# Kernel tuning notes

Hardware: AMD Instinct MI355X
Metric: run time of the kernel (lower is better)

Reference implementation:

```python
import jax, jax.numpy as jnp
import numpy as np

LINHAS, COLUNAS, DIM, BATCH = 64, 64, 512, 256
N_NEURONS = LINHAS * COLUNAS
TAXA_INICIAL = 0.5
SIGMA_INICIAL = max(LINHAS, COLUNAS) / 2.0  # 32.0


def _grid_locations():
    # Matches tf.meshgrid (default 'xy' indexing) -> stack -> reshape(-1, 2)
    x = jnp.arange(LINHAS, dtype=jnp.float32)
    y = jnp.arange(COLUNAS, dtype=jnp.float32)
    gx, gy = jnp.meshgrid(x, y)  # 'xy' indexing, shapes (COLUNAS, LINHAS)
    return jnp.stack([gx, gy], axis=-1).reshape(-1, 2)  # (N_NEURONS, 2)


def setup_inputs() -> dict:
    key = jax.random.key(0)
    kx, kw = jax.random.split(key)
    X = jax.random.normal(kx, (BATCH, DIM), dtype=jnp.float32)
    # keras 'random_normal' initializer: stddev 0.05
    pesos = jax.random.normal(kw, (N_NEURONS, DIM), dtype=jnp.float32) * 0.05
    return {
        "X": X,
        "pesos": pesos,
        "localizacoes": _grid_locations(),
        "passo_atual": 10,
        "total_passos": 1000,
    }


def reference(X, pesos, localizacoes, passo_atual, total_passos):
    decay = jnp.exp(jnp.float32(-passo_atual / total_passos))
    taxa = TAXA_INICIAL * decay
    sigma = SIGMA_INICIAL * decay

    # Euclidean cdist^2: (B, N)
    x2 = jnp.sum(X * X, axis=1, keepdims=True)            # (B, 1)
    w2 = jnp.sum(pesos * pesos, axis=1)                   # (N,)
    dist = x2 + w2 - 2.0 * (X @ pesos.T)                  # (B, N)

    bmu_idx = jnp.argmin(dist, axis=1)                    # (B,)
    bmu_loc = localizacoes[bmu_idx]                       # (B, 2)

    # Squared grid distance from every neuron to each sample's BMU: (B, N)
    diff = localizacoes[None, :, :] - bmu_loc[:, None, :]
    dist_grade = jnp.sum(diff * diff, axis=2)
    h = jnp.exp(-dist_grade / (2.0 * sigma * sigma))      # (B, N)

    # delta_total[n, d] = taxa * mean_b h[b, n] * (X[b, d] - pesos[n, d])
    # computed without materializing the (B, N, D) delta tensor.
    B = jnp.float32(X.shape[0])
    hX = jnp.einsum("bn,bd->nd", h, X)                    # (N, D)
    h_sum = jnp.sum(h, axis=0)                            # (N,)
    delta_total = (taxa / B) * (hX - h_sum[:, None] * pesos)

    new_pesos = pesos + delta_total
    return new_pesos, taxa, sigma
```

## Files before the change

kernel.cpp:

```cpp
#include <hip/hip_runtime.h>
#include <hip/hip_bf16.h>

typedef unsigned int u32;
typedef unsigned short u16;
typedef unsigned long long u64;

#define BATCH 256
#define NN 4096
#define DIM 512

using short8 = __attribute__((ext_vector_type(8))) short;
using f32x4  = __attribute__((ext_vector_type(4))) float;

__device__ inline float b2f(u16 u){ u32 i = ((u32)u)<<16; float f; __builtin_memcpy(&f,&i,4); return f; }
__device__ inline u16 f2b(float v){ __hip_bfloat16 h = __float2bfloat16(v); u16 r; __builtin_memcpy(&r,&h,2); return r; }

__device__ inline float ldv(const void* p, size_t i, int isbf){
  return isbf ? b2f(((const u16*)p)[i]) : ((const float*)p)[i];
}
__device__ inline void stv(void* p, size_t i, float v, int isbf){
  if (isbf) ((__hip_bfloat16*)p)[i] = __float2bfloat16(v);
  else ((float*)p)[i] = v;
}

__device__ inline int sniff(const void* X, int t, int* sh){
  if (t < 64){
    u32 v = ((const u32*)X)[t];
    u16 lo = (u16)(v & 0xffffu);
    int e = (lo >> 7) & 0xff;
    int sane = ((lo & 0x7fffu) == 0) || (e >= 110 && e <= 132);
    u64 m = __ballot(sane);
    if (t == 0) *sh = (__popcll(m) >= 32) ? 1 : 0;
  }
  __syncthreads();
  return *sh;
}

__global__ __launch_bounds__(256) void k_prep(const void* X, const void* W,
    u64* pack, float* w2, u16* XT, u16* Xb, u16* Wb,
    const int* passo, const int* total, void* out){
  __shared__ int sflag;
  __shared__ u32 sT[64][33];
  int t = threadIdx.x;
  int isbf = sniff(X, t, &sflag);
  int blk = blockIdx.x;
  if (blk < 32){
    int td = blk & 7, tb = blk >> 3;
    #pragma unroll
    for (int it=0; it<8; ++it){
      int i = it*256 + t;
      int r = i>>5, cc = i&31;
      size_t gi = (size_t)(tb*64 + r)*DIM + td*64 + cc*2;
      u32 v;
      if (isbf){
        v = *(const u32*)((const u16*)X + gi);
      } else {
        float2 f = *(const float2*)((const float*)X + gi);
        v = (u32)f2b(f.x) | ((u32)f2b(f.y) << 16);
        *(u32*)(Xb + gi) = v;
      }
      sT[r][cc] = v;
    }
    __syncthreads();
    #pragma unroll
    for (int it=0; it<8; ++it){
      int i = it*256 + t;
      int dd = i>>5, bb2 = i&31;
      u32 lo = sT[bb2*2][dd>>1], hi = sT[bb2*2+1][dd>>1];
      int sh = (dd&1)*16;
      u32 v = ((lo >> sh) & 0xffffu) | (((hi >> sh) & 0xffffu) << 16);
      *(u32*)(XT + (size_t)(td*64+dd)*BATCH + tb*64 + bb2*2) = v;
    }
  } else {
    int j = blk - 32;
    int n0 = j*8;
    int wv = t>>6, lane = t&63;
    #pragma unroll
    for (int rr=0; rr<2; ++rr){
      int n = n0 + wv*2 + rr;
      float xv[8]; float s = 0.f;
      if (isbf){
        short8 x = *(const short8*)((const u16*)W + (size_t)n*DIM + lane*8);
        #pragma unroll
        for (int q=0;q<8;q++) xv[q] = b2f((u16)x[q]);
      } else {
        #pragma unroll
        for (int q=0;q<8;q++) xv[q] = ((const float*)W)[(size_t)n*DIM + lane*8 + q];
      }
      #pragma unroll
      for (int q=0;q<8;q++) s += xv[q]*xv[q];
      #pragma unroll
      for (int off=32; off; off>>=1) s += __shfl_down(s, off);
      if (lane == 0) w2[n] = s;
      if (!isbf){
        #pragma unroll
        for (int q=0;q<8;q++) Wb[(size_t)n*DIM + lane*8 + q] = f2b(xv[q]);
      }
    }
    if (j == 0){
      pack[t] = ~0ull;
      if (t == 0){
        float decay = expf(-(float)passo[0]/(float)total[0]);
        stv(out, (size_t)NN*DIM,     0.5f*decay, isbf);
        stv(out, (size_t)NN*DIM + 1, 32.f*decay, isbf);
      }
    }
  }
}

__global__ __launch_bounds__(256) void k_score(const void* X, const void* W,
    const u16* Xws, const u16* Wws, const float* w2, u64* pack){
  __shared__ int sflag;
  __shared__ float sval[4][32];
  __shared__ int   sidx[4][32];
  int t = threadIdx.x;
  int isbf = sniff(X, t, &sflag);
  const u16* Xb = isbf ? (const u16*)X : Xws;
  const u16* Wb = isbf ? (const u16*)W : Wws;
  int wv = t>>6, l = t&63;
  int lr = l&15, lg = l>>4;

  int id = blockIdx.x;
  int xcd = id & 7, sub = id >> 3;
  int ny = xcd*4 + (sub>>3);
  int bx = sub & 7;
  int b0 = bx*32;
  int n0 = ny*128 + wv*32;

  const u16* xp0 = Xb + (size_t)(b0 + lr)*DIM + lg*8;
  const u16* xp1 = xp0 + (size_t)16*DIM;
  const u16* wp0 = Wb + (size_t)(n0 + lr)*DIM + lg*8;
  const u16* wp1 = wp0 + (size_t)16*DIM;

  f32x4 acc00 = {0,0,0,0}, acc01 = {0,0,0,0}, acc10 = {0,0,0,0}, acc11 = {0,0,0,0};
  #pragma unroll
  for (int ks=0; ks<16; ++ks){
    short8 a0 = *(const short8*)(xp0 + ks*32);
    short8 a1 = *(const short8*)(xp1 + ks*32);
    short8 w0 = *(const short8*)(wp0 + ks*32);
    short8 w1 = *(const short8*)(wp1 + ks*32);
    acc00 = __builtin_amdgcn_mfma_f32_16x16x32_bf16(a0, w0, acc00, 0,0,0);
    acc01 = __builtin_amdgcn_mfma_f32_16x16x32_bf16(a0, w1, acc01, 0,0,0);
    acc10 = __builtin_amdgcn_mfma_f32_16x16x32_bf16(a1, w0, acc10, 0,0,0);
    acc11 = __builtin_amdgcn_mfma_f32_16x16x32_bf16(a1, w1, acc11, 0,0,0);
  }

  float w20 = w2[n0 + lr];
  float w21 = w2[n0 + 16 + lr];
  #pragma unroll
  for (int bb=0; bb<2; ++bb){
    #pragma unroll
    for (int r=0;r<4;++r){
      float s0 = w20 - 2.f*(bb ? acc10[r] : acc00[r]);
      float s1 = w21 - 2.f*(bb ? acc11[r] : acc01[r]);
      float bv; int bi;
      if (s0 <= s1){ bv = s0; bi = n0 + lr; } else { bv = s1; bi = n0 + 16 + lr; }
      #pragma unroll
      for (int m=1; m<16; m<<=1){
        float ov = __shfl_xor(bv, m);
        int   oi = __shfl_xor(bi, m);
        if (ov < bv || (ov == bv && oi < bi)){ bv = ov; bi = oi; }
      }
      if (lr == 0){ int bl = bb*16 + lg*4 + r; sval[wv][bl] = bv; sidx[wv][bl] = bi; }
    }
  }
  __syncthreads();
  if (t < 32){
    float bv = sval[0][t]; int bi = sidx[0][t];
    #pragma unroll
    for (int w4=1; w4<4; ++w4){
      float ov = sval[w4][t]; int oi = sidx[w4][t];
      if (ov < bv || (ov == bv && oi < bi)){ bv = ov; bi = oi; }
    }
    u32 sb = __float_as_uint(bv);
    sb = (sb & 0x80000000u) ? ~sb : (sb | 0x80000000u);
    atomicMin(pack + b0 + t, ((u64)sb << 32) | (u32)bi);
  }
}

__global__ __launch_bounds__(512) void k_update(const void* X, const u16* XT, const void* W,
    const u64* pack, const int* passo, const int* total, void* out){
  __shared__ int sflag;
  __shared__ u16 hT[16][264];
  __shared__ float hpart[8][8];
  __shared__ float hs[16];
  int t = threadIdx.x;
  int isbf = sniff(X, t, &sflag);
  int wv = t>>6, l = t&63;
  int n0 = blockIdx.x * 16;

  float decay = expf(-(float)passo[0] / (float)total[0]);
  float taxa = 0.5f*decay, sigma = 32.f*decay;
  float inv2s2 = 1.f/(2.f*sigma*sigma);

  {
    int b = t & 255;
    int rbase = (t >> 8) * 8;
    int m = (int)(u32)(pack[b] & 0xffffffffu);
    int mx = m & 63, my = m >> 6;
    float hv[8];
    #pragma unroll
    for (int i=0;i<8;++i){
      int n = n0 + rbase + i;
      int dx = (n & 63) - mx;
      int dy = (n >> 6) - my;
      float h = expf(-(float)(dx*dx + dy*dy) * inv2s2);
      hv[i] = h;
      hT[rbase + i][b] = f2b(h);
    }
    #pragma unroll
    for (int i=0;i<8;++i){
      float s = hv[i];
      #pragma unroll
      for (int off=32; off; off>>=1) s += __shfl_down(s, off);
      if (l == 0) hpart[wv][i] = s;
    }
  }
  __syncthreads();
  if (t < 16){
    int g = (t >> 3) * 4;
    hs[t] = hpart[g][t&7] + hpart[g+1][t&7] + hpart[g+2][t&7] + hpart[g+3][t&7];
  }
  __syncthreads();

  int lr = l & 15, lg = l >> 4;
  int d0 = wv * 64;
  f32x4 acc[4];
  #pragma unroll
  for (int f=0;f<4;++f) acc[f] = (f32x4){0.f,0.f,0.f,0.f};

  #pragma unroll
  for (int ks=0; ks<8; ++ks){
    short8 a = *(const short8*)(&hT[lr][ks*32 + lg*8]);
    #pragma unroll
    for (int f=0; f<4; ++f){
      short8 bfr = *(const short8*)(XT + (size_t)(d0 + f*16 + lr)*BATCH + ks*32 + lg*8);
      acc[f] = __builtin_amdgcn_mfma_f32_16x16x32_bf16(a, bfr, acc[f], 0,0,0);
    }
  }

  float cc = taxa / (float)BATCH;
  #pragma unroll
  for (int r=0;r<4;++r){
    int n = n0 + lg*4 + r;
    float hsv = hs[lg*4 + r];
    #pragma unroll
    for (int f=0;f<4;++f){
      size_t gi = (size_t)n*DIM + d0 + f*16 + lr;
      float wv_ = ldv(W, gi, isbf);
      float o = wv_ + cc*(acc[f][r] - hsv*wv_);
      stv(out, gi, o, isbf);
    }
  }
}

extern "C" void kernel_launch(void* const* d_in, const int* in_sizes, int n_in,
                              void* d_out, int out_size, void* d_ws, size_t ws_size,
                              hipStream_t stream) {
  const void* X = d_in[0];
  const void* W = d_in[1];
  const int* passo = (const int*)d_in[3];
  const int* total = (const int*)d_in[4];

  char* ws = (char*)d_ws;
  u64* pack = (u64*)(ws + 256);
  float* w2 = (float*)(ws + 2304);
  u16* XT   = (u16*)(ws + 18688);
  u16* Xb   = (u16*)(ws + 280832);
  u16* Wb   = (u16*)(ws + 542976);

  k_prep  <<<544, 256, 0, stream>>>(X, W, pack, w2, XT, Xb, Wb, passo, total, d_out);
  k_score <<<256, 256, 0, stream>>>(X, W, Xb, Wb, w2, pack);
  k_update<<<256, 512, 0, stream>>>(X, XT, W, pack, passo, total, d_out);
}
```

Before: 41.49 us.

## Split score GEMM over K across waves and compute weight norms inline

The scoring kernel now launches 512 blocks of 512 threads. Each wave computes a 16x32 tile over half of the K dimension, and the two K-halves are reduced through shared memory. The squared weight norms are computed from the bf16 weight fragments already loaded for the MFMA, so the w2 array is no longer read. The aim is more parallelism and latency hiding in the score pass, at the cost of a shared-memory reduction and extra block sync. The w2 values now come from bf16-rounded weights, which differs slightly from the fp32 norms and could change argmin ties. k_prep still writes w2.

After: 43.07 us. 3.8% more time.

```diff
diff --git a/kernel.cpp b/kernel.cpp
--- a/kernel.cpp
+++ b/kernel.cpp
@@ -108,51 +108,63 @@
   }
 }
 
-__global__ __launch_bounds__(256) void k_score(const void* X, const void* W,
-    const u16* Xws, const u16* Wws, const float* w2, u64* pack){
+__global__ __launch_bounds__(512) void k_score(const void* X, const void* W,
+    const u16* Xws, const u16* Wws, u64* pack){
   __shared__ int sflag;
-  __shared__ float sval[4][32];
-  __shared__ int   sidx[4][32];
+  __shared__ float pf[4][64][10];
+  __shared__ float sval[2][32];
+  __shared__ int   sidx[2][32];
   int t = threadIdx.x;
   int isbf = sniff(X, t, &sflag);
-  const u16* Xb = isbf ? (const u16*)X : Xws;
-  const u16* Wb = isbf ? (const u16*)W : Wws;
-  int wv = t>>6, l = t&63;
-  int lr = l&15, lg = l>>4;
+  const u16* Xp = isbf ? (const u16*)X : Xws;
+  const u16* Wp = isbf ? (const u16*)W : Wws;
+  int wv = t>>6, l = t&63, lr = l&15, lg = l>>4;
+  int bh = wv&1, nh = (wv>>1)&1, kh = wv>>2;
 
   int id = blockIdx.x;
   int xcd = id & 7, sub = id >> 3;
-  int ny = xcd*4 + (sub>>3);
-  int bx = sub & 7;
-  int b0 = bx*32;
-  int n0 = ny*128 + wv*32;
-
-  const u16* xp0 = Xb + (size_t)(b0 + lr)*DIM + lg*8;
-  const u16* xp1 = xp0 + (size_t)16*DIM;
-  const u16* wp0 = Wb + (size_t)(n0 + lr)*DIM + lg*8;
+  int nc = xcd*8 + (sub>>3);
+  int bt = sub & 7;
+  int b0 = bt*32 + bh*16;
+  int n0 = nc*64 + nh*32;
+  int k0 = kh*256;
+
+  const u16* xp  = Xp + (size_t)(b0 + lr)*DIM + k0 + lg*8;
+  const u16* wp0 = Wp + (size_t)(n0 + lr)*DIM + k0 + lg*8;
   const u16* wp1 = wp0 + (size_t)16*DIM;
 
-  f32x4 acc00 = {0,0,0,0}, acc01 = {0,0,0,0}, acc10 = {0,0,0,0}, acc11 = {0,0,0,0};
-  #pragma unroll
-  for (int ks=0; ks<16; ++ks){
-    short8 a0 = *(const short8*)(xp0 + ks*32);
-    short8 a1 = *(const short8*)(xp1 + ks*32);
+  f32x4 acc0 = {0,0,0,0}, acc1 = {0,0,0,0};
+  float sq0 = 0.f, sq1 = 0.f;
+  #pragma unroll
+  for (int ks=0; ks<8; ++ks){
+    short8 a  = *(const short8*)(xp  + ks*32);
     short8 w0 = *(const short8*)(wp0 + ks*32);
     short8 w1 = *(const short8*)(wp1 + ks*32);
-    acc00 = __builtin_amdgcn_mfma_f32_16x16x32_bf16(a0, w0, acc00, 0,0,0);
-    acc01 = __builtin_amdgcn_mfma_f32_16x16x32_bf16(a0, w1, acc01, 0,0,0);
-    acc10 = __builtin_amdgcn_mfma_f32_16x16x32_bf16(a1, w0, acc10, 0,0,0);
-    acc11 = __builtin_amdgcn_mfma_f32_16x16x32_bf16(a1, w1, acc11, 0,0,0);
-  }
-
-  float w20 = w2[n0 + lr];
-  float w21 = w2[n0 + 16 + lr];
-  #pragma unroll
-  for (int bb=0; bb<2; ++bb){
+    acc0 = __builtin_amdgcn_mfma_f32_16x16x32_bf16(a, w0, acc0, 0,0,0);
+    acc1 = __builtin_amdgcn_mfma_f32_16x16x32_bf16(a, w1, acc1, 0,0,0);
+    #pragma unroll
+    for (int q=0;q<8;++q){
+      float f0 = b2f((u16)w0[q]); sq0 = fmaf(f0, f0, sq0);
+      float f1 = b2f((u16)w1[q]); sq1 = fmaf(f1, f1, sq1);
+    }
+  }
+  sq0 += __shfl_xor(sq0, 16); sq0 += __shfl_xor(sq0, 32);
+  sq1 += __shfl_xor(sq1, 16); sq1 += __shfl_xor(sq1, 32);
+
+  if (kh){
+    #pragma unroll
+    for (int r=0;r<4;++r){ pf[wv-4][l][r] = acc0[r]; pf[wv-4][l][4+r] = acc1[r]; }
+    pf[wv-4][l][8] = sq0; pf[wv-4][l][9] = sq1;
+  }
+  __syncthreads();
+  if (!kh){
+    #pragma unroll
+    for (int r=0;r<4;++r){ acc0[r] += pf[wv][l][r]; acc1[r] += pf[wv][l][4+r]; }
+    sq0 += pf[wv][l][8]; sq1 += pf[wv][l][9];
     #pragma unroll
     for (int r=0;r<4;++r){
-      float s0 = w20 - 2.f*(bb ? acc10[r] : acc00[r]);
-      float s1 = w21 - 2.f*(bb ? acc11[r] : acc01[r]);
+      float s0 = sq0 - 2.f*acc0[r];
+      float s1 = sq1 - 2.f*acc1[r];
       float bv; int bi;
       if (s0 <= s1){ bv = s0; bi = n0 + lr; } else { bv = s1; bi = n0 + 16 + lr; }
       #pragma unroll
@@ -161,20 +173,20 @@
         int   oi = __shfl_xor(bi, m);
         if (ov < bv || (ov == bv && oi < bi)){ bv = ov; bi = oi; }
       }
-      if (lr == 0){ int bl = bb*16 + lg*4 + r; sval[wv][bl] = bv; sidx[wv][bl] = bi; }
+      if (lr == 0){
+        sval[nh][bh*16 + lg*4 + r] = bv;
+        sidx[nh][bh*16 + lg*4 + r] = bi;
+      }
     }
   }
   __syncthreads();
   if (t < 32){
     float bv = sval[0][t]; int bi = sidx[0][t];
-    #pragma unroll
-    for (int w4=1; w4<4; ++w4){
-      float ov = sval[w4][t]; int oi = sidx[w4][t];
-      if (ov < bv || (ov == bv && oi < bi)){ bv = ov; bi = oi; }
-    }
+    float ov = sval[1][t]; int oi = sidx[1][t];
+    if (ov < bv || (ov == bv && oi < bi)){ bv = ov; bi = oi; }
     u32 sb = __float_as_uint(bv);
     sb = (sb & 0x80000000u) ? ~sb : (sb | 0x80000000u);
-    atomicMin(pack + b0 + t, ((u64)sb << 32) | (u32)bi);
+    atomicMin(pack + bt*32 + t, ((u64)sb << 32) | (u32)bi);
   }
 }
 
@@ -270,6 +282,6 @@
   u16* Wb   = (u16*)(ws + 542976);
 
   k_prep  <<<544, 256, 0, stream>>>(X, W, pack, w2, XT, Xb, Wb, passo, total, d_out);
-  k_score <<<256, 256, 0, stream>>>(X, W, Xb, Wb, w2, pack);
+  k_score <<<512, 512, 0, stream>>>(X, W, Xb, Wb, pack);
   k_update<<<256, 512, 0, stream>>>(X, XT, W, pack, passo, total, d_out);
 }
```
